# Kernel tuning notes

Hardware: AMD Instinct MI355X
Metric: run time of the kernel (lower is better)

## Reference

```python
import jax, jax.numpy as jnp
import numpy as np

B, S, D_IN, D_H = 8, 2048, 1024, 1024
LR = 0.01  # inner-loop SGD learning rate


def setup_inputs() -> dict:
    key = jax.random.key(0)
    ks = jax.random.split(key, 6)
    return {
        "in_seq": jax.random.normal(ks[0], (B, S, D_IN), jnp.float32),
        "theta_K": jax.random.normal(ks[1], (D_H, D_IN), jnp.float32) * 0.02,
        "theta_V": jax.random.normal(ks[2], (D_H, D_IN), jnp.float32) * 0.02,
        "theta_Q": jax.random.normal(ks[3], (D_H, D_IN), jnp.float32) * 0.02,
        "W0": jax.random.normal(ks[4], (D_H, D_H), jnp.float32) * 0.02,  # inner linear init
        "b0": jnp.zeros((D_H,), jnp.float32),
    }


def reference(in_seq, theta_K, theta_V, theta_Q, W0, b0):
    """TTT layer: per-token inner SGD step on MSE(W@k+b, v), then predict W@q+b."""
    d_h = W0.shape[0]
    # Precompute all three views in big batched GEMMs: [B,S,D_H]
    K = jnp.einsum('bsd,ed->bse', in_seq, theta_K)
    V = jnp.einsum('bsd,ed->bse', in_seq, theta_V)
    Q = jnp.einsum('bsd,ed->bse', in_seq, theta_Q)

    def step(carry, kvq):
        W, b = carry
        k, v, q = kvq
        pred = W @ k + b                      # inner model forward on train view
        g = (2.0 / d_h) * (pred - v)          # d(MSE)/d(pred), MSE = mean over d_h
        W = W - LR * jnp.outer(g, k)          # SGD step: grad_W = g k^T
        b = b - LR * g                        # grad_b = g
        out = W @ q + b                       # predict with updated weights
        return (W, b), out

    def run_seq(k_s, v_s, q_s):
        _, ys = jax.lax.scan(step, (W0, b0), (k_s, v_s, q_s))
        return ys  # [S, D_H]

    return jax.vmap(run_seq)(K, V, Q)  # [B, S, D_H]
```

## Files before the change

kernel.cpp:

```cpp
#include <hip/hip_runtime.h>
#include <hip/hip_bf16.h>

#define LR 0.01f

typedef __attribute__((ext_vector_type(8))) short short8;
typedef __attribute__((ext_vector_type(4))) float float4v;
typedef __attribute__((ext_vector_type(4))) unsigned short ushort4v;

static __device__ __forceinline__ unsigned short f2bf(float x) {
    union { float f; unsigned u; } un; un.f = x;
    unsigned r = un.u + 0x7fffu + ((un.u >> 16) & 1u);
    return (unsigned short)(r >> 16);
}
static __device__ __forceinline__ float bf2f(unsigned short x) {
    union { float f; unsigned u; } un; un.u = ((unsigned)x) << 16;
    return un.f;
}

__global__ __launch_bounds__(256) void cast_all(
    const float* __restrict__ A,
    const float* __restrict__ T0, const float* __restrict__ T1,
    const float* __restrict__ T2,
    unsigned short* __restrict__ Ab,
    unsigned short* __restrict__ Tb)
{
    const int bid = blockIdx.x;
    const int tid = threadIdx.x;
    if (bid < 2048) {
        for (int i = bid * 256 + tid; i < 2097152; i += 2048 * 256) {
            const float4v* s = (const float4v*)(A + (size_t)i * 8);
            float4v a = s[0], b = s[1];
            short8 o;
#pragma unroll
            for (int j = 0; j < 4; ++j) { o[j] = (short)f2bf(a[j]); o[j + 4] = (short)f2bf(b[j]); }
            *(short8*)(Ab + (size_t)i * 8) = o;
        }
    } else {
        const int base = bid - 2048;
        const int t = base >> 7;
        const int lb = base & 127;
        const float* S = (t == 0) ? T0 : (t == 1 ? T1 : T2);
        unsigned short* D = Tb + (size_t)t * 1048576;
        for (int i = lb * 256 + tid; i < 131072; i += 128 * 256) {
            const float4v* s = (const float4v*)(S + (size_t)i * 8);
            float4v a = s[0], b = s[1];
            short8 o;
#pragma unroll
            for (int j = 0; j < 4; ++j) { o[j] = (short)f2bf(a[j]); o[j + 4] = (short)f2bf(b[j]); }
            *(short8*)(D + (size_t)i * 8) = o;
        }
    }
}

__global__ __launch_bounds__(256) void proj_gemm_bf(
    const unsigned short* __restrict__ A,
    const unsigned short* __restrict__ Tb,
    unsigned short* __restrict__ out,
    unsigned short* __restrict__ ktw)
{
    __shared__ unsigned short As[64][40];
    __shared__ unsigned short Bs[3][64][40];

    const int tid  = threadIdx.x;
    const int lane = tid & 63;
    const int wave = tid >> 6;
    const int m0 = blockIdx.x * 64;
    const int n0 = blockIdx.y * 64;
    const int srow = tid >> 2;
    const int sseg = (tid & 3) * 8;
    const int mrow = lane & 15;
    const int quad = lane >> 4;

    float4v acc[3][4];
#pragma unroll
    for (int z = 0; z < 3; ++z)
#pragma unroll
        for (int i = 0; i < 4; ++i) acc[z][i] = (float4v){0.f, 0.f, 0.f, 0.f};

    const unsigned short* apBase = A  + (size_t)(m0 + srow) * 1024 + sseg;
    const unsigned short* bp0 = Tb               + (size_t)(n0 + srow) * 1024 + sseg;
    const unsigned short* bp1 = Tb + 1048576     + (size_t)(n0 + srow) * 1024 + sseg;
    const unsigned short* bp2 = Tb + 2 * 1048576 + (size_t)(n0 + srow) * 1024 + sseg;

    for (int kt = 0; kt < 1024; kt += 32) {
        short8 av = *(const short8*)(apBase + kt);
        short8 b0 = *(const short8*)(bp0 + kt);
        short8 b1 = *(const short8*)(bp1 + kt);
        short8 b2 = *(const short8*)(bp2 + kt);

        __syncthreads();
        *(short8*)&As[srow][sseg]    = av;
        *(short8*)&Bs[0][srow][sseg] = b0;
        *(short8*)&Bs[1][srow][sseg] = b1;
        *(short8*)&Bs[2][srow][sseg] = b2;
        __syncthreads();

        short8 af = *(const short8*)&As[16 * wave + mrow][quad * 8];
#pragma unroll
        for (int z = 0; z < 3; ++z)
#pragma unroll
            for (int nb = 0; nb < 4; ++nb) {
                short8 bfr = *(const short8*)&Bs[z][16 * nb + mrow][quad * 8];
                acc[z][nb] = __builtin_amdgcn_mfma_f32_16x16x32_bf16(af, bfr, acc[z][nb], 0, 0, 0);
            }
    }

    const int batch = m0 >> 11;
    const int s0    = m0 & 2047;
#pragma unroll
    for (int z = 0; z < 3; ++z) {
        unsigned short* C = out + (size_t)z * (size_t)16384 * 1024;
#pragma unroll
        for (int nb = 0; nb < 4; ++nb) {
#pragma unroll
            for (int r = 0; r < 4; ++r) {
                int tl = 16 * wave + quad * 4 + r;
                int jl = 16 * nb + mrow;
                C[(size_t)(m0 + tl) * 1024 + (n0 + jl)] = f2bf(acc[z][nb][r]);
                if (z == 0) {
                    ktw[(size_t)batch * 2097152 + (size_t)(n0 + jl) * 2048 + s0 + tl] =
                        f2bf(-LR * acc[0][nb][r]);
                }
            }
        }
    }
}

__global__ __launch_bounds__(256) void proj_gemm(
    const float* __restrict__ A,
    const float* __restrict__ T0, const float* __restrict__ T1,
    const float* __restrict__ T2,
    unsigned short* __restrict__ out,
    unsigned short* __restrict__ ktw)
{
    __shared__ unsigned short As[64][40];
    __shared__ unsigned short Bs[3][64][40];

    const int tid  = threadIdx.x;
    const int lane = tid & 63;
    const int wave = tid >> 6;
    const int m0 = blockIdx.x * 64;
    const int n0 = blockIdx.y * 64;
    const int srow = tid >> 2;
    const int sseg = (tid & 3) * 8;
    const int mrow = lane & 15;
    const int quad = lane >> 4;

    float4v acc[3][4];
#pragma unroll
    for (int z = 0; z < 3; ++z)
#pragma unroll
        for (int i = 0; i < 4; ++i) acc[z][i] = (float4v){0.f, 0.f, 0.f, 0.f};

    const float* apBase = A  + (size_t)(m0 + srow) * 1024 + sseg;
    const float* bp0 = T0 + (size_t)(n0 + srow) * 1024 + sseg;
    const float* bp1 = T1 + (size_t)(n0 + srow) * 1024 + sseg;
    const float* bp2 = T2 + (size_t)(n0 + srow) * 1024 + sseg;

    for (int kt = 0; kt < 1024; kt += 32) {
        float4v av0 = ((const float4v*)(apBase + kt))[0];
        float4v av1 = ((const float4v*)(apBase + kt))[1];
        float4v b00 = ((const float4v*)(bp0 + kt))[0], b01 = ((const float4v*)(bp0 + kt))[1];
        float4v b10 = ((const float4v*)(bp1 + kt))[0], b11 = ((const float4v*)(bp1 + kt))[1];
        float4v b20 = ((const float4v*)(bp2 + kt))[0], b21 = ((const float4v*)(bp2 + kt))[1];

        __syncthreads();
        short8 apk, bpk0, bpk1, bpk2;
#pragma unroll
        for (int i = 0; i < 4; ++i) {
            apk[i]      = (short)f2bf(av0[i]);
            apk[i + 4]  = (short)f2bf(av1[i]);
            bpk0[i]     = (short)f2bf(b00[i]);
            bpk0[i + 4] = (short)f2bf(b01[i]);
            bpk1[i]     = (short)f2bf(b10[i]);
            bpk1[i + 4] = (short)f2bf(b11[i]);
            bpk2[i]     = (short)f2bf(b20[i]);
            bpk2[i + 4] = (short)f2bf(b21[i]);
        }
        *(short8*)&As[srow][sseg]    = apk;
        *(short8*)&Bs[0][srow][sseg] = bpk0;
        *(short8*)&Bs[1][srow][sseg] = bpk1;
        *(short8*)&Bs[2][srow][sseg] = bpk2;
        __syncthreads();

        short8 af = *(const short8*)&As[16 * wave + mrow][quad * 8];
#pragma unroll
        for (int z = 0; z < 3; ++z)
#pragma unroll
            for (int nb = 0; nb < 4; ++nb) {
                short8 bfr = *(const short8*)&Bs[z][16 * nb + mrow][quad * 8];
                acc[z][nb] = __builtin_amdgcn_mfma_f32_16x16x32_bf16(af, bfr, acc[z][nb], 0, 0, 0);
            }
    }

    const int batch = m0 >> 11;
    const int s0    = m0 & 2047;
#pragma unroll
    for (int z = 0; z < 3; ++z) {
        unsigned short* C = out + (size_t)z * (size_t)16384 * 1024;
#pragma unroll
        for (int nb = 0; nb < 4; ++nb) {
#pragma unroll
            for (int r = 0; r < 4; ++r) {
                int tl = 16 * wave + quad * 4 + r;
                int jl = 16 * nb + mrow;
                C[(size_t)(m0 + tl) * 1024 + (n0 + jl)] = f2bf(acc[z][nb][r]);
                if (z == 0) {
                    ktw[(size_t)batch * 2097152 + (size_t)(n0 + jl) * 2048 + s0 + tl] =
                        f2bf(-LR * acc[0][nb][r]);
                }
            }
        }
    }
}

__global__ __launch_bounds__(256) void precomp(
    const unsigned short* __restrict__ K,
    const unsigned short* __restrict__ Q,
    unsigned short* __restrict__ LinvG,
    unsigned short* __restrict__ MpG)
{
    __shared__ float Skk[64][68];
    __shared__ float Sqk[64][68];
    __shared__ unsigned short Lb[64][72];
    __shared__ unsigned short Xa[64][72];

    const int tid = threadIdx.x;
    const int lane = tid & 63;
    const int w = tid >> 6;
    const int lm = lane & 15;
    const int quad = lane >> 4;
    const int batch = blockIdx.x >> 5;
    const int c = blockIdx.x & 31;
    const size_t blk = (size_t)batch * 32 + c;

    float4v kk[4], qk[4];
#pragma unroll
    for (int i = 0; i < 4; ++i) { kk[i] = (float4v){0,0,0,0}; qk[i] = (float4v){0,0,0,0}; }

    const size_t tokA = (size_t)batch * 2048 + c * 64 + w * 16 + lm;
#pragma unroll 4
    for (int ks = 0; ks < 32; ++ks) {
        short8 aK = *(const short8*)(K + tokA * 1024 + ks * 32 + quad * 8);
        short8 aQ = *(const short8*)(Q + tokA * 1024 + ks * 32 + quad * 8);
#pragma unroll
        for (int nb = 0; nb < 4; ++nb) {
            size_t tokB = (size_t)batch * 2048 + c * 64 + nb * 16 + lm;
            short8 bK = *(const short8*)(K + tokB * 1024 + ks * 32 + quad * 8);
            kk[nb] = __builtin_amdgcn_mfma_f32_16x16x32_bf16(aK, bK, kk[nb], 0, 0, 0);
            qk[nb] = __builtin_amdgcn_mfma_f32_16x16x32_bf16(aQ, bK, qk[nb], 0, 0, 0);
        }
    }
#pragma unroll
    for (int nb = 0; nb < 4; ++nb)
#pragma unroll
        for (int r = 0; r < 4; ++r) {
            Skk[w * 16 + quad * 4 + r][nb * 16 + lm] = kk[nb][r];
            Sqk[w * 16 + quad * 4 + r][nb * 16 + lm] = qk[nb][r];
        }
    __syncthreads();

    const float c1 = 2.0f * LR / 1024.0f;
#pragma unroll
    for (int e = 0; e < 16; ++e) {
        int idx = tid * 16 + e;
        int t = idx >> 6, i = idx & 63;
        float a = (i < t) ? c1 * (Skk[t][i] + 1.0f) : 0.0f;
        Lb[t][i] = f2bf(a);
        Xa[i][t] = f2bf(((i == t) ? 1.0f : 0.0f) - a);
        float mq = (i <= t) ? -LR * (Sqk[t][i] + 1.0f) : 0.0f;
        MpG[blk * 4096 + (size_t)t * 64 + i] = f2bf(mq);
    }
    __syncthreads();

    short8 afL0 = *(const short8*)&Lb[w * 16 + lm][quad * 8];
    short8 afL1 = *(const short8*)&Lb[w * 16 + lm][32 + quad * 8];
    float4v p[4];
#pragma unroll
    for (int nb = 0; nb < 4; ++nb) {
        p[nb] = (float4v){0,0,0,0};
        short8 b0f = *(const short8*)&Xa[nb * 16 + lm][quad * 8];
        short8 b1f = *(const short8*)&Xa[nb * 16 + lm][32 + quad * 8];
        p[nb] = __builtin_amdgcn_mfma_f32_16x16x32_bf16(afL0, b0f, p[nb], 0, 0, 0);
        p[nb] = __builtin_amdgcn_mfma_f32_16x16x32_bf16(afL1, b1f, p[nb], 0, 0, 0);
    }
    __syncthreads();
#pragma unroll
    for (int nb = 0; nb < 4; ++nb)
#pragma unroll
        for (int r = 0; r < 4; ++r) {
            int ii = nb * 16 + lm, tt = w * 16 + quad * 4 + r;
            Xa[ii][tt] = f2bf(((ii == tt) ? 1.0f : 0.0f) - p[nb][r]);
        }
    __syncthreads();

#pragma unroll
    for (int nb = 0; nb < 4; ++nb) {
        p[nb] = (float4v){0,0,0,0};
        short8 b0f = *(const short8*)&Xa[nb * 16 + lm][quad * 8];
        short8 b1f = *(const short8*)&Xa[nb * 16 + lm][32 + quad * 8];
        p[nb] = __builtin_amdgcn_mfma_f32_16x16x32_bf16(afL0, b0f, p[nb], 0, 0, 0);
        p[nb] = __builtin_amdgcn_mfma_f32_16x16x32_bf16(afL1, b1f, p[nb], 0, 0, 0);
    }
#pragma unroll
    for (int nb = 0; nb < 4; ++nb)
#pragma unroll
        for (int r = 0; r < 4; ++r) {
            int ii = nb * 16 + lm, tt = w * 16 + quad * 4 + r;
            LinvG[blk * 4096 + (size_t)tt * 64 + ii] =
                f2bf(((ii == tt) ? 1.0f : 0.0f) - p[nb][r]);
        }
}

__global__ __launch_bounds__(512, 2) void ttt_chunk(
    const unsigned short* __restrict__ K,
    const unsigned short* __restrict__ V,
    const unsigned short* __restrict__ Q,
    const unsigned short* __restrict__ Kt,
    const unsigned short* __restrict__ Linv,
    const unsigned short* __restrict__ Mp,
    const float* __restrict__ W0,
    const float* __restrict__ b0,
    float* __restrict__ out)
{
    __shared__ unsigned short Wb[32][1032];
    __shared__ unsigned short Ut[32][72];
    __shared__ unsigned short Gt[32][72];
    __shared__ __align__(16) float bb[32];

    const int tid  = threadIdx.x;
    const int lane = tid & 63;
    const int w    = tid >> 6;
    const int g    = w & 3;
    const int role = w >> 2;
    const int lm   = lane & 15;
    const int quad = lane >> 4;
    const int batch = blockIdx.x & 7;
    const int r0    = (blockIdx.x >> 3) * 32;

    float4v acc_w[2][8];
#pragma unroll
    for (int rs2 = 0; rs2 < 2; ++rs2)
#pragma unroll
        for (int i = 0; i < 8; ++i) {
            int nt = w + 8 * i;
#pragma unroll
            for (int r = 0; r < 4; ++r)
                acc_w[rs2][i][r] =
                    W0[(size_t)(r0 + rs2 * 16 + quad * 4 + r) * 1024 + nt * 16 + lm];
        }
    if (tid < 32) bb[tid] = b0[r0 + tid];

    const size_t tokBase = (size_t)batch * 2048;
    const unsigned short* KtB = Kt + (size_t)batch * 2097152;
    const unsigned short* X = role ? Q : K;
    const float sc = 2.0f / 1024.0f;

    for (int c = 0; c < 32; ++c) {
#pragma unroll
        for (int rs2 = 0; rs2 < 2; ++rs2)
#pragma unroll
            for (int i = 0; i < 8; ++i) {
                int nt = w + 8 * i;
#pragma unroll
                for (int r = 0; r < 4; ++r)
                    Wb[rs2 * 16 + quad * 4 + r][nt * 16 + lm] = f2bf(acc_w[rs2][i][r]);
            }
        __syncthreads();

        const size_t tok = tokBase + c * 64 + g * 16 + lm;
        const unsigned short* xRow  = X + tok * 1024 + quad * 8;
        const unsigned short* wRow0 = &Wb[lm][quad * 8];
        const unsigned short* wRow1 = &Wb[16 + lm][quad * 8];
        float4v a0v = (float4v){0,0,0,0};
        float4v a1v = (float4v){0,0,0,0};
#pragma unroll 8
        for (int ks = 0; ks < 32; ++ks) {
            short8 xf  = *(const short8*)(xRow + ks * 32);
            short8 af0 = *(const short8*)(wRow0 + ks * 32);
            short8 af1 = *(const short8*)(wRow1 + ks * 32);
            a0v = __builtin_amdgcn_mfma_f32_16x16x32_bf16(af0, xf, a0v, 0, 0, 0);
            a1v = __builtin_amdgcn_mfma_f32_16x16x32_bf16(af1, xf, a1v, 0, 0, 0);
        }
        float4v bval0 = *(const float4v*)&bb[quad * 4];
        float4v bval1 = *(const float4v*)&bb[16 + quad * 4];
        if (role == 0) {
            ushort4v vv0 = *(const ushort4v*)(V + tok * 1024 + r0 + quad * 4);
            ushort4v vv1 = *(const ushort4v*)(V + tok * 1024 + r0 + 16 + quad * 4);
#pragma unroll
            for (int r = 0; r < 4; ++r) {
                Ut[quad * 4 + r][g * 16 + lm]      = f2bf(sc * (a0v[r] + bval0[r] - bf2f(vv0[r])));
                Ut[16 + quad * 4 + r][g * 16 + lm] = f2bf(sc * (a1v[r] + bval1[r] - bf2f(vv1[r])));
            }
        }
        __syncthreads();

        const size_t lbase = ((size_t)(batch * 32 + c)) * 4096 + (size_t)(g * 16 + lm) * 64;

        {
            float4v accG = (float4v){0,0,0,0};
            short8 a0 = *(const short8*)&Ut[role * 16 + lm][quad * 8];
            short8 a1 = *(const short8*)&Ut[role * 16 + lm][32 + quad * 8];
            short8 l0 = *(const short8*)(Linv + lbase + quad * 8);
            short8 l1 = *(const short8*)(Linv + lbase + 32 + quad * 8);
            accG = __builtin_amdgcn_mfma_f32_16x16x32_bf16(a0, l0, accG, 0, 0, 0);
            accG = __builtin_amdgcn_mfma_f32_16x16x32_bf16(a1, l1, accG, 0, 0, 0);
#pragma unroll
            for (int r = 0; r < 4; ++r)
                Gt[role * 16 + quad * 4 + r][g * 16 + lm] = f2bf(accG[r]);
        }
        __syncthreads();

        short8 agA0 = *(const short8*)&Gt[lm][quad * 8];
        short8 agA1 = *(const short8*)&Gt[lm][32 + quad * 8];
        short8 agB0 = *(const short8*)&Gt[16 + lm][quad * 8];
        short8 agB1 = *(const short8*)&Gt[16 + lm][32 + quad * 8];

        if (role == 1) {
            short8 m0f = *(const short8*)(Mp + lbase + quad * 8);
            short8 m1f = *(const short8*)(Mp + lbase + 32 + quad * 8);
            a0v = __builtin_amdgcn_mfma_f32_16x16x32_bf16(agA0, m0f, a0v, 0, 0, 0);
            a0v = __builtin_amdgcn_mfma_f32_16x16x32_bf16(agA1, m1f, a0v, 0, 0, 0);
            a1v = __builtin_amdgcn_mfma_f32_16x16x32_bf16(agB0, m0f, a1v, 0, 0, 0);
            a1v = __builtin_amdgcn_mfma_f32_16x16x32_bf16(agB1, m1f, a1v, 0, 0, 0);
            float4v ov0, ov1;
#pragma unroll
            for (int r = 0; r < 4; ++r) { ov0[r] = a0v[r] + bval0[r]; ov1[r] = a1v[r] + bval1[r]; }
            *(float4v*)(out + tok * 1024 + r0 + quad * 4)      = ov0;
            *(float4v*)(out + tok * 1024 + r0 + 16 + quad * 4) = ov1;
        }

#pragma unroll
        for (int i = 0; i < 8; ++i) {
            int nt = w + 8 * i;
            const unsigned short* kp = KtB + (size_t)(nt * 16 + lm) * 2048 + c * 64;
            short8 kb0 = *(const short8*)(kp + quad * 8);
            short8 kb1 = *(const short8*)(kp + 32 + quad * 8);
            acc_w[0][i] = __builtin_amdgcn_mfma_f32_16x16x32_bf16(agA0, kb0, acc_w[0][i], 0, 0, 0);
            acc_w[0][i] = __builtin_amdgcn_mfma_f32_16x16x32_bf16(agA1, kb1, acc_w[0][i], 0, 0, 0);
            acc_w[1][i] = __builtin_amdgcn_mfma_f32_16x16x32_bf16(agB0, kb0, acc_w[1][i], 0, 0, 0);
            acc_w[1][i] = __builtin_amdgcn_mfma_f32_16x16x32_bf16(agB1, kb1, acc_w[1][i], 0, 0, 0);
        }

        if (w == 0) {
            int row = lane >> 1, part = lane & 1;
            float s = 0.f;
#pragma unroll
            for (int t = 0; t < 32; ++t) s += bf2f(Gt[row][part * 32 + t]);
            s += __shfl_xor(s, 1);
            if (part == 0) bb[row] -= LR * s;
        }
        __syncthreads();
    }
}

extern "C" void kernel_launch(void* const* d_in, const int* in_sizes, int n_in,
                              void* d_out, int out_size, void* d_ws, size_t ws_size,
                              hipStream_t stream) {
    (void)in_sizes; (void)n_in; (void)out_size;
    const float* in_seq = (const float*)d_in[0];
    const float* thK    = (const float*)d_in[1];
    const float* thV    = (const float*)d_in[2];
    const float* thQ    = (const float*)d_in[3];
    const float* W0     = (const float*)d_in[4];
    const float* b0     = (const float*)d_in[5];
    float* out = (float*)d_out;

    unsigned short* ws = (unsigned short*)d_ws;
    unsigned short* Kp   = ws;
    unsigned short* Vp   = ws + (size_t)16384 * 1024;
    unsigned short* Qp   = ws + (size_t)2 * 16384 * 1024;
    unsigned short* Ktp  = ws + (size_t)3 * 16384 * 1024;
    unsigned short* Linv = ws + (size_t)4 * 16384 * 1024;
    unsigned short* Mpp  = Linv + (size_t)8 * 32 * 4096;
    unsigned short* Abf  = Mpp + (size_t)8 * 32 * 4096;
    unsigned short* Tbf  = Abf + (size_t)16384 * 1024;

    const size_t need_shorts = (size_t)4 * 16384 * 1024 + 2 * (size_t)8 * 32 * 4096
                             + (size_t)16384 * 1024 + (size_t)3 * 1024 * 1024;

    dim3 g1(16384 / 64, 1024 / 64);
    if (ws_size >= need_shorts * 2) {
        cast_all<<<2432, 256, 0, stream>>>(in_seq, thK, thV, thQ, Abf, Tbf);
        proj_gemm_bf<<<g1, 256, 0, stream>>>(Abf, Tbf, Kp, Ktp);
    } else {
        proj_gemm<<<g1, 256, 0, stream>>>(in_seq, thK, thV, thQ, Kp, Ktp);
    }

    precomp<<<256, 256, 0, stream>>>(Kp, Qp, Linv, Mpp);

    ttt_chunk<<<256, 512, 0, stream>>>(Kp, Vp, Qp, Ktp, Linv, Mpp, W0, b0, out);
}
```

Before: 766.7 us.

## Store K and Q in MFMA fragment-tiled layout for contiguous operand loads

The projection GEMM now writes K and Q in a layout that matches the 16x16x32 MFMA B-operand fragments (64-token chunk, 16-row group, 32-column k-step, then lane-contiguous 8 elements). The precomp and ttt_chunk kernels read these fragments with one contiguous 16-byte load per lane, so each wave touches a contiguous 1 KB region instead of 16 rows spaced by the row stride. V and the transposed K copy keep their old layout. The epilogue's scattered 2-byte stores become more irregular, which may raise write cost in the projection kernel.

```diff
diff --git a/kernel.cpp b/kernel.cpp
--- a/kernel.cpp
+++ b/kernel.cpp
@@ -15,6 +15,11 @@
 static __device__ __forceinline__ float bf2f(unsigned short x) {
     union { float f; unsigned u; } un; un.u = ((unsigned)x) << 16;
     return un.f;
+}
+
+static __device__ __forceinline__ size_t kq_frag_idx(int b, int s, int j) {
+    return ((((size_t)(b * 32 + (s >> 6)) * 4 + ((s >> 4) & 3)) * 32 + (j >> 5)) * 512)
+         + (size_t)(((j >> 3) & 3) * 16 + (s & 15)) * 8 + (j & 7);
 }
 
 __global__ __launch_bounds__(256) void cast_all(
@@ -55,7 +60,9 @@
 __global__ __launch_bounds__(256) void proj_gemm_bf(
     const unsigned short* __restrict__ A,
     const unsigned short* __restrict__ Tb,
-    unsigned short* __restrict__ out,
+    unsigned short* __restrict__ Kf,
+    unsigned short* __restrict__ Vp,
+    unsigned short* __restrict__ Qf,
     unsigned short* __restrict__ ktw)
 {
     __shared__ unsigned short As[64][40];
@@ -108,20 +115,18 @@
     const int batch = m0 >> 11;
     const int s0    = m0 & 2047;
 #pragma unroll
-    for (int z = 0; z < 3; ++z) {
-        unsigned short* C = out + (size_t)z * (size_t)16384 * 1024;
-#pragma unroll
-        for (int nb = 0; nb < 4; ++nb) {
-#pragma unroll
-            for (int r = 0; r < 4; ++r) {
-                int tl = 16 * wave + quad * 4 + r;
-                int jl = 16 * nb + mrow;
-                C[(size_t)(m0 + tl) * 1024 + (n0 + jl)] = f2bf(acc[z][nb][r]);
-                if (z == 0) {
-                    ktw[(size_t)batch * 2097152 + (size_t)(n0 + jl) * 2048 + s0 + tl] =
-                        f2bf(-LR * acc[0][nb][r]);
-                }
-            }
+    for (int nb = 0; nb < 4; ++nb) {
+#pragma unroll
+        for (int r = 0; r < 4; ++r) {
+            int tl = 16 * wave + quad * 4 + r;
+            int jl = 16 * nb + mrow;
+            int s = s0 + tl;
+            int j = n0 + jl;
+            size_t fK = kq_frag_idx(batch, s, j);
+            Kf[fK] = f2bf(acc[0][nb][r]);
+            Qf[fK] = f2bf(acc[2][nb][r]);
+            Vp[(size_t)(m0 + tl) * 1024 + j] = f2bf(acc[1][nb][r]);
+            ktw[(size_t)batch * 2097152 + (size_t)j * 2048 + s] = f2bf(-LR * acc[0][nb][r]);
         }
     }
 }
@@ -130,7 +135,9 @@
     const float* __restrict__ A,
     const float* __restrict__ T0, const float* __restrict__ T1,
     const float* __restrict__ T2,
-    unsigned short* __restrict__ out,
+    unsigned short* __restrict__ Kf,
+    unsigned short* __restrict__ Vp,
+    unsigned short* __restrict__ Qf,
     unsigned short* __restrict__ ktw)
 {
     __shared__ unsigned short As[64][40];
@@ -196,20 +203,18 @@
     const int batch = m0 >> 11;
     const int s0    = m0 & 2047;
 #pragma unroll
-    for (int z = 0; z < 3; ++z) {
-        unsigned short* C = out + (size_t)z * (size_t)16384 * 1024;
-#pragma unroll
-        for (int nb = 0; nb < 4; ++nb) {
-#pragma unroll
-            for (int r = 0; r < 4; ++r) {
-                int tl = 16 * wave + quad * 4 + r;
-                int jl = 16 * nb + mrow;
-                C[(size_t)(m0 + tl) * 1024 + (n0 + jl)] = f2bf(acc[z][nb][r]);
-                if (z == 0) {
-                    ktw[(size_t)batch * 2097152 + (size_t)(n0 + jl) * 2048 + s0 + tl] =
-                        f2bf(-LR * acc[0][nb][r]);
-                }
-            }
+    for (int nb = 0; nb < 4; ++nb) {
+#pragma unroll
+        for (int r = 0; r < 4; ++r) {
+            int tl = 16 * wave + quad * 4 + r;
+            int jl = 16 * nb + mrow;
+            int s = s0 + tl;
+            int j = n0 + jl;
+            size_t fK = kq_frag_idx(batch, s, j);
+            Kf[fK] = f2bf(acc[0][nb][r]);
+            Qf[fK] = f2bf(acc[2][nb][r]);
+            Vp[(size_t)(m0 + tl) * 1024 + j] = f2bf(acc[1][nb][r]);
+            ktw[(size_t)batch * 2097152 + (size_t)j * 2048 + s] = f2bf(-LR * acc[0][nb][r]);
         }
     }
 }
@@ -238,15 +243,15 @@
 #pragma unroll
     for (int i = 0; i < 4; ++i) { kk[i] = (float4v){0,0,0,0}; qk[i] = (float4v){0,0,0,0}; }
 
-    const size_t tokA = (size_t)batch * 2048 + c * 64 + w * 16 + lm;
+    const unsigned short* aKp = K + (blk * 4 + w) * 16384 + (size_t)lane * 8;
+    const unsigned short* aQp = Q + (blk * 4 + w) * 16384 + (size_t)lane * 8;
 #pragma unroll 4
     for (int ks = 0; ks < 32; ++ks) {
-        short8 aK = *(const short8*)(K + tokA * 1024 + ks * 32 + quad * 8);
-        short8 aQ = *(const short8*)(Q + tokA * 1024 + ks * 32 + quad * 8);
+        short8 aK = *(const short8*)(aKp + ks * 512);
+        short8 aQ = *(const short8*)(aQp + ks * 512);
 #pragma unroll
         for (int nb = 0; nb < 4; ++nb) {
-            size_t tokB = (size_t)batch * 2048 + c * 64 + nb * 16 + lm;
-            short8 bK = *(const short8*)(K + tokB * 1024 + ks * 32 + quad * 8);
+            short8 bK = *(const short8*)(K + (blk * 4 + nb) * 16384 + (size_t)lane * 8 + ks * 512);
             kk[nb] = __builtin_amdgcn_mfma_f32_16x16x32_bf16(aK, bK, kk[nb], 0, 0, 0);
             qk[nb] = __builtin_amdgcn_mfma_f32_16x16x32_bf16(aQ, bK, qk[nb], 0, 0, 0);
         }
@@ -369,14 +374,15 @@
         __syncthreads();
 
         const size_t tok = tokBase + c * 64 + g * 16 + lm;
-        const unsigned short* xRow  = X + tok * 1024 + quad * 8;
+        const unsigned short* xRow =
+            X + (((size_t)batch * 32 + c) * 4 + g) * 16384 + (size_t)lane * 8;
         const unsigned short* wRow0 = &Wb[lm][quad * 8];
         const unsigned short* wRow1 = &Wb[16 + lm][quad * 8];
         float4v a0v = (float4v){0,0,0,0};
         float4v a1v = (float4v){0,0,0,0};
 #pragma unroll 8
         for (int ks = 0; ks < 32; ++ks) {
-            short8 xf  = *(const short8*)(xRow + ks * 32);
+            short8 xf  = *(const short8*)(xRow + ks * 512);
             short8 af0 = *(const short8*)(wRow0 + ks * 32);
             short8 af1 = *(const short8*)(wRow1 + ks * 32);
             a0v = __builtin_amdgcn_mfma_f32_16x16x32_bf16(af0, xf, a0v, 0, 0, 0);
@@ -467,9 +473,9 @@
     float* out = (float*)d_out;
 
     unsigned short* ws = (unsigned short*)d_ws;
-    unsigned short* Kp   = ws;
+    unsigned short* Kf   = ws;
     unsigned short* Vp   = ws + (size_t)16384 * 1024;
-    unsigned short* Qp   = ws + (size_t)2 * 16384 * 1024;
+    unsigned short* Qf   = ws + (size_t)2 * 16384 * 1024;
     unsigned short* Ktp  = ws + (size_t)3 * 16384 * 1024;
     unsigned short* Linv = ws + (size_t)4 * 16384 * 1024;
     unsigned short* Mpp  = Linv + (size_t)8 * 32 * 4096;
@@ -482,12 +488,12 @@
     dim3 g1(16384 / 64, 1024 / 64);
     if (ws_size >= need_shorts * 2) {
         cast_all<<<2432, 256, 0, stream>>>(in_seq, thK, thV, thQ, Abf, Tbf);
-        proj_gemm_bf<<<g1, 256, 0, stream>>>(Abf, Tbf, Kp, Ktp);
+        proj_gemm_bf<<<g1, 256, 0, stream>>>(Abf, Tbf, Kf, Vp, Qf, Ktp);
     } else {
-        proj_gemm<<<g1, 256, 0, stream>>>(in_seq, thK, thV, thQ, Kp, Ktp);
-    }
-
-    precomp<<<256, 256, 0, stream>>>(Kp, Qp, Linv, Mpp);
-
-    ttt_chunk<<<256, 512, 0, stream>>>(Kp, Vp, Qp, Ktp, Linv, Mpp, W0, b0, out);
-}
+        proj_gemm<<<g1, 256, 0, stream>>>(in_seq, thK, thV, thQ, Kf, Vp, Qf, Ktp);
+    }
+
+    precomp<<<256, 256, 0, stream>>>(Kf, Qf, Linv, Mpp);
+
+    ttt_chunk<<<256, 512, 0, stream>>>(Kf, Vp, Qf, Ktp, Linv, Mpp, W0, b0, out);
+}
```

Result: slower. 800.2 us (+4.4%).
